# Kernel tuning notes

Hardware: AMD Instinct MI355X
Metric: run time of the kernel (lower is better)

Reference implementation:

```python
import jax, jax.numpy as jnp
import numpy as np

B, S, C = 4, 8192, 256        # batch, seq len, channels
NW, WS, PSZ, D = 2048, 256, 256, 32  # words, word_size, p_size, window radius


def setup_inputs() -> dict:
    key = jax.random.key(0)
    k0, k1, k2, k3, k4 = jax.random.split(key, 5)
    q = jax.random.normal(k0, (B, S, C), jnp.float32)
    c_t = jax.random.normal(k1, (B, NW, WS), jnp.float32)
    # scale weights ~1/sqrt(fan_in) so sigmoid in predictive alignment is not saturated
    W_a = jax.random.normal(k2, (WS, C), jnp.float32) / np.sqrt(C).astype(np.float32)
    W_p = jax.random.normal(k3, (PSZ, WS), jnp.float32) / np.sqrt(WS).astype(np.float32)
    V_p = jax.random.normal(k4, (1, PSZ), jnp.float32) / np.sqrt(PSZ).astype(np.float32)
    return {"q": q, "c_t": c_t, "W_a": W_a, "W_p": W_p, "V_p": V_p}


def reference(q, c_t, W_a, W_p, V_p):
    Bq, Sq, Cq = q.shape
    # predictive alignment: p_t = S * sigmoid(V_p(tanh(W_p(c_t))))  -> [B, NW, 1]
    p_t = Sq * jax.nn.sigmoid(jnp.tanh(c_t @ W_p.T) @ V_p.T)
    # window positions s in [p-D, p+D]; torch .long() truncates (p_t > 0 so == floor)
    offs = jnp.arange(-D, D + 1)                       # [K]
    s = p_t[..., 0].astype(jnp.int32)[:, :, None] + offs  # [B, NW, K]
    # pad a leading NaN row; out-of-range indices map to it (clamp then mod)
    q_pad = jnp.concatenate([jnp.full((Bq, 1, Cq), jnp.nan, q.dtype), q], axis=1)  # [B, S+1, C]
    idx = jnp.clip(s + 1, 0, Sq + 1) % (Sq + 1)        # S+1 wraps to the NaN row (0)
    qw = jax.vmap(lambda qb, ib: qb[ib])(q_pad, idx)   # [B, NW, K, C] gathered windows
    nan_mask = jnp.isnan(qw[..., 0])                   # [B, NW, K]
    qw = jnp.where(nan_mask[..., None], 0.0, qw)       # zero invalid keys (used for output too)
    Wq = qw @ W_a.T                                    # [B, NW, K, WS]
    a_t = jnp.einsum('bwkd,bwd->bwk', Wq, c_t)         # per-window scores
    a_t = jnp.where(nan_mask, -jnp.inf, a_t)           # NaN keys -> -inf before softmax
    prob = jax.nn.softmax(a_t, axis=2)
    # Gaussian truncation around predicted position p_t
    prob = prob * jnp.exp(-2.0 * jnp.square((s.astype(q.dtype) - p_t) / D))
    out = jnp.einsum('bwk,bwkc->bwc', prob, qw)        # [B, NW, C]
    return out
```

## Files before the change

kernel.cpp:

```cpp
#include <hip/hip_runtime.h>
#include <math.h>

#define BB 4
#define S 8192
#define C 256
#define NW 2048
#define WS 256
#define PSZ 256
#define DD 32
#define KK 65
#define TOTW (BB * NW)

#define KC 64
#define LDA 68
#define NBKT 64
#define TBKT (BB * NBKT)

__global__ __launch_bounds__(256) void prep_B(const float* __restrict__ Wp,
                                              const float* __restrict__ Wa,
                                              float* __restrict__ Bp,
                                              int* __restrict__ cnt) {
    const int k = blockIdx.x;
    const int t = threadIdx.x;
    Bp[k * 512 + t] = Wp[t * WS + k];
    Bp[k * 512 + 256 + t] = Wa[k * C + t];
    if (k == 0) cnt[t] = 0;
}

__global__ __launch_bounds__(256, 4) void precomp_gemm(const float* __restrict__ ct,
                                                       const float* __restrict__ Bp,
                                                       const float* __restrict__ Vp,
                                                       float* __restrict__ ptpart,
                                                       float* __restrict__ g) {
    __shared__ __align__(16) float Al[KC][LDA];
    __shared__ __align__(16) float Bl[KC][LDA];

    const int t = threadIdx.x;
    const int bm = blockIdx.x >> 3;
    const int bn = blockIdx.x & 7;
    const int tm = t >> 4;
    const int tn = t & 15;
    const int sm = t >> 2;
    const int sf = t & 3;

    const float4* ct4 = (const float4*)ct;
    const float4* B4  = (const float4*)Bp;

    float acc[4][4] = {{0.f}};

    for (int kc = 0; kc < 256; kc += KC) {
        __syncthreads();
#pragma unroll
        for (int i = 0; i < 4; i++) {
            const float4 a = ct4[(size_t)(bm * 64 + sm) * 64 + (kc >> 2) + sf + i * 4];
            const int kl = (sf + i * 4) * 4;
            Al[kl + 0][sm] = a.x;
            Al[kl + 1][sm] = a.y;
            Al[kl + 2][sm] = a.z;
            Al[kl + 3][sm] = a.w;
        }
#pragma unroll
        for (int i = 0; i < 4; i++) {
            const float4 b = B4[(size_t)(kc + sm) * 128 + bn * 16 + sf + i * 4];
            *(float4*)&Bl[sm][(sf + i * 4) * 4] = b;
        }
        __syncthreads();

#pragma unroll 8
        for (int kk = 0; kk < KC; kk++) {
            const float4 a = *(const float4*)&Al[kk][tm * 4];
            const float4 b = *(const float4*)&Bl[kk][tn * 4];
            acc[0][0] = fmaf(a.x, b.x, acc[0][0]);
            acc[0][1] = fmaf(a.x, b.y, acc[0][1]);
            acc[0][2] = fmaf(a.x, b.z, acc[0][2]);
            acc[0][3] = fmaf(a.x, b.w, acc[0][3]);
            acc[1][0] = fmaf(a.y, b.x, acc[1][0]);
            acc[1][1] = fmaf(a.y, b.y, acc[1][1]);
            acc[1][2] = fmaf(a.y, b.z, acc[1][2]);
            acc[1][3] = fmaf(a.y, b.w, acc[1][3]);
            acc[2][0] = fmaf(a.z, b.x, acc[2][0]);
            acc[2][1] = fmaf(a.z, b.y, acc[2][1]);
            acc[2][2] = fmaf(a.z, b.z, acc[2][2]);
            acc[2][3] = fmaf(a.z, b.w, acc[2][3]);
            acc[3][0] = fmaf(a.w, b.x, acc[3][0]);
            acc[3][1] = fmaf(a.w, b.y, acc[3][1]);
            acc[3][2] = fmaf(a.w, b.z, acc[3][2]);
            acc[3][3] = fmaf(a.w, b.w, acc[3][3]);
        }
    }

    if (bn >= 4) {
        const int col = bn * 64 + tn * 4 - 256;
#pragma unroll
        for (int i = 0; i < 4; i++) {
            const int row = bm * 64 + tm * 4 + i;
            *(float4*)&g[(size_t)row * 256 + col] =
                make_float4(acc[i][0], acc[i][1], acc[i][2], acc[i][3]);
        }
    } else {
        const float4 vp4 = ((const float4*)Vp)[bn * 16 + tn];
#pragma unroll
        for (int i = 0; i < 4; i++) {
            float v = tanhf(acc[i][0]) * vp4.x;
            v = fmaf(tanhf(acc[i][1]), vp4.y, v);
            v = fmaf(tanhf(acc[i][2]), vp4.z, v);
            v = fmaf(tanhf(acc[i][3]), vp4.w, v);
#pragma unroll
            for (int off = 8; off >= 1; off >>= 1) v += __shfl_xor(v, off);
            if (tn == 0) {
                const int row = bm * 64 + tm * 4 + i;
                ptpart[row * 4 + bn] = v;
            }
        }
    }
}

__global__ __launch_bounds__(256) void pt_hist(const float* __restrict__ ptpart,
                                               float* __restrict__ pt,
                                               int* __restrict__ cnt) {
    const int wg = blockIdx.x * 256 + threadIdx.x;
    const float4 pp = ((const float4*)ptpart)[wg];
    const float x = (pp.x + pp.y) + (pp.z + pp.w);
    const float p = (float)S / (1.f + expf(-x));
    pt[wg] = p;
    const int s0 = (int)p;
    const int bkt = (wg >> 11) * NBKT + min(NBKT - 1, max(0, s0 >> 7));
    atomicAdd(&cnt[bkt], 1);
}

__global__ __launch_bounds__(256) void scan_kernel(const int* __restrict__ cnt,
                                                   int* __restrict__ offs) {
    __shared__ int sh[TBKT];
    const int t = threadIdx.x;
    const int v = cnt[t];
    sh[t] = v;
    __syncthreads();
    for (int d = 1; d < TBKT; d <<= 1) {
        const int x = (t >= d) ? sh[t - d] : 0;
        __syncthreads();
        sh[t] += x;
        __syncthreads();
    }
    offs[t] = sh[t] - v;
}

__global__ __launch_bounds__(256) void scatter_kernel(const float* __restrict__ pt,
                                                      int* __restrict__ offs,
                                                      int* __restrict__ perm) {
    const int wg = blockIdx.x * 256 + threadIdx.x;
    const int s0 = (int)pt[wg];
    const int bkt = (wg >> 11) * NBKT + min(NBKT - 1, max(0, s0 >> 7));
    const int pos = atomicAdd(&offs[bkt], 1);
    perm[pos] = wg;
}

__global__ __launch_bounds__(256, 3) void attn(const float* __restrict__ q,
                                               const float* __restrict__ g,
                                               const float* __restrict__ pt,
                                               const int* __restrict__ perm,
                                               float* __restrict__ out) {
    __shared__ __align__(16) float4 accbuf[4][64];
    __shared__ float mbuf[4], dbuf[4];

    const int tid = threadIdx.x;
    const int l = tid & 63;
    const int wv = tid >> 6;
    const int gw = l >> 4;
    const int sub = l & 15;
    const int kslot = tid >> 4;

    const int bid = blockIdx.x;
    const int sb = (bid & 7) * 1024 + (bid >> 3);
    const int wg = perm[sb];
    const int b = wg >> 11;

    const float p = pt[wg];
    const int s0 = (int)p;

    const float* grow = g + (size_t)wg * C + sub * 4;
    const float4 g0 = *(const float4*)(grow);
    const float4 g1 = *(const float4*)(grow + 64);
    const float4 g2 = *(const float4*)(grow + 128);
    const float4 g3 = *(const float4*)(grow + 192);

    const float* qb = q + (size_t)b * S * C + sub * 4;

    float4 qh[5][4];
#pragma unroll
    for (int it = 0; it < 5; it++) {
        const int s = s0 + it * 16 + kslot - DD;
        const float* qr = qb + (size_t)min(max(s, 0), S - 1) * C;
        qh[it][0] = *(const float4*)(qr);
        qh[it][1] = *(const float4*)(qr + 64);
        qh[it][2] = *(const float4*)(qr + 128);
        qh[it][3] = *(const float4*)(qr + 192);
    }

    float e[5];
#pragma unroll
    for (int it = 0; it < 5; it++) {
        const int k = it * 16 + kslot;
        const int s = s0 + k - DD;
        const bool valid = (k <= 64) && ((unsigned)s < (unsigned)S);
        float d0 = qh[it][0].x * g0.x, d1 = qh[it][1].x * g1.x;
        float d2 = qh[it][2].x * g2.x, d3 = qh[it][3].x * g3.x;
        d0 = fmaf(qh[it][0].y, g0.y, d0); d1 = fmaf(qh[it][1].y, g1.y, d1);
        d2 = fmaf(qh[it][2].y, g2.y, d2); d3 = fmaf(qh[it][3].y, g3.y, d3);
        d0 = fmaf(qh[it][0].z, g0.z, d0); d1 = fmaf(qh[it][1].z, g1.z, d1);
        d2 = fmaf(qh[it][2].z, g2.z, d2); d3 = fmaf(qh[it][3].z, g3.z, d3);
        d0 = fmaf(qh[it][0].w, g0.w, d0); d1 = fmaf(qh[it][1].w, g1.w, d1);
        d2 = fmaf(qh[it][2].w, g2.w, d2); d3 = fmaf(qh[it][3].w, g3.w, d3);
        float d = (d0 + d1) + (d2 + d3);
#pragma unroll
        for (int off = 8; off >= 1; off >>= 1) d += __shfl_xor(d, off);
        e[it] = valid ? d : -3e38f;
    }

    float m = e[0];
#pragma unroll
    for (int it = 1; it < 5; it++) m = fmaxf(m, e[it]);
    m = fmaxf(m, __shfl_xor(m, 16));
    m = fmaxf(m, __shfl_xor(m, 32));

    float den = 0.f;
#pragma unroll
    for (int it = 0; it < 5; it++) {
        e[it] = __expf(e[it] - m);
        den += e[it];
    }
    den += __shfl_xor(den, 16);
    den += __shfl_xor(den, 32);

#pragma unroll
    for (int it = 0; it < 5; it++) {
        const float fs = (float)(s0 + it * 16 + kslot - DD) - p;
        const float tt = fs * (1.f / (float)DD);
        e[it] *= __expf(-2.f * tt * tt);
    }

    float4 a0 = {0,0,0,0}, a1 = {0,0,0,0}, a2 = {0,0,0,0}, a3 = {0,0,0,0};
#pragma unroll
    for (int it = 0; it < 5; it++) {
        const float w = e[it];
        a0.x = fmaf(w, qh[it][0].x, a0.x); a0.y = fmaf(w, qh[it][0].y, a0.y);
        a0.z = fmaf(w, qh[it][0].z, a0.z); a0.w = fmaf(w, qh[it][0].w, a0.w);
        a1.x = fmaf(w, qh[it][1].x, a1.x); a1.y = fmaf(w, qh[it][1].y, a1.y);
        a1.z = fmaf(w, qh[it][1].z, a1.z); a1.w = fmaf(w, qh[it][1].w, a1.w);
        a2.x = fmaf(w, qh[it][2].x, a2.x); a2.y = fmaf(w, qh[it][2].y, a2.y);
        a2.z = fmaf(w, qh[it][2].z, a2.z); a2.w = fmaf(w, qh[it][2].w, a2.w);
        a3.x = fmaf(w, qh[it][3].x, a3.x); a3.y = fmaf(w, qh[it][3].y, a3.y);
        a3.z = fmaf(w, qh[it][3].z, a3.z); a3.w = fmaf(w, qh[it][3].w, a3.w);
    }

#define MERGE(v) { v += __shfl_xor(v, 16); v += __shfl_xor(v, 32); }
    MERGE(a0.x) MERGE(a0.y) MERGE(a0.z) MERGE(a0.w)
    MERGE(a1.x) MERGE(a1.y) MERGE(a1.z) MERGE(a1.w)
    MERGE(a2.x) MERGE(a2.y) MERGE(a2.z) MERGE(a2.w)
    MERGE(a3.x) MERGE(a3.y) MERGE(a3.z) MERGE(a3.w)
#undef MERGE

    float4 o = a0;
    if (gw == 1) o = a1;
    else if (gw == 2) o = a2;
    else if (gw == 3) o = a3;
    accbuf[wv][l] = o;
    if (l == 0) { mbuf[wv] = m; dbuf[wv] = den; }
    __syncthreads();

    if (tid < 64) {
        const float M = fmaxf(fmaxf(mbuf[0], mbuf[1]), fmaxf(mbuf[2], mbuf[3]));
        const float sc0 = __expf(mbuf[0] - M);
        const float sc1 = __expf(mbuf[1] - M);
        const float sc2 = __expf(mbuf[2] - M);
        const float sc3 = __expf(mbuf[3] - M);
        const float dtot = dbuf[0]*sc0 + dbuf[1]*sc1 + dbuf[2]*sc2 + dbuf[3]*sc3;
        const float4 v0 = accbuf[0][tid];
        const float4 v1 = accbuf[1][tid];
        const float4 v2 = accbuf[2][tid];
        const float4 v3 = accbuf[3][tid];
        const float r = 1.f / dtot;
        float4 oo;
        oo.x = (v0.x*sc0 + v1.x*sc1 + v2.x*sc2 + v3.x*sc3) * r;
        oo.y = (v0.y*sc0 + v1.y*sc1 + v2.y*sc2 + v3.y*sc3) * r;
        oo.z = (v0.z*sc0 + v1.z*sc1 + v2.z*sc2 + v3.z*sc3) * r;
        oo.w = (v0.w*sc0 + v1.w*sc1 + v2.w*sc2 + v3.w*sc3) * r;
        *(float4*)(out + (size_t)wg * C + tid * 4) = oo;
    }
}

extern "C" void kernel_launch(void* const* d_in, const int* in_sizes, int n_in,
                              void* d_out, int out_size, void* d_ws, size_t ws_size,
                              hipStream_t stream) {
    const float* q  = (const float*)d_in[0];
    const float* ct = (const float*)d_in[1];
    const float* Wa = (const float*)d_in[2];
    const float* Wp = (const float*)d_in[3];
    const float* Vp = (const float*)d_in[4];
    float* out = (float*)d_out;

    char* ws = (char*)d_ws;
    float* Bp     = (float*)ws;
    float* ptpart = (float*)(ws + 524288);
    float* pt     = (float*)(ws + 655360);
    int*   cnt    = (int*)  (ws + 688128);
    int*   offs   = (int*)  (ws + 689152);
    int*   perm   = (int*)  (ws + 690176);
    float* g      = (float*)(ws + 722944);

    prep_B<<<256, 256, 0, stream>>>(Wp, Wa, Bp, cnt);
    precomp_gemm<<<1024, 256, 0, stream>>>(ct, Bp, Vp, ptpart, g);
    pt_hist<<<TOTW / 256, 256, 0, stream>>>(ptpart, pt, cnt);
    scan_kernel<<<1, TBKT, 0, stream>>>(cnt, offs);
    scatter_kernel<<<TOTW / 256, 256, 0, stream>>>(pt, offs, perm);
    attn<<<TOTW, 256, 0, stream>>>(q, g, pt, perm, out);
}
```

Baseline: 88.65 us.

## Fuse histogram, scan and scatter into one single-block sort kernel

Replaces the three bucket-sort kernels (global-atomic histogram, scan, scatter) with one single-workgroup kernel that builds the histogram in LDS, scans it, and scatters the permutation. Global counters and their zeroing in prep_B go away, which removes two kernel launches and the global-atomic traffic. The cost is that 8192 items are now processed by a single block serially. The attention kernel's occupancy hint is also lowered from 3 to 2 blocks per CU, and row pointers are kept in an array, presumably for reuse later in the kernel.

```diff
diff --git a/kernel.cpp b/kernel.cpp
--- a/kernel.cpp
+++ b/kernel.cpp
@@ -18,13 +18,11 @@
 
 __global__ __launch_bounds__(256) void prep_B(const float* __restrict__ Wp,
                                               const float* __restrict__ Wa,
-                                              float* __restrict__ Bp,
-                                              int* __restrict__ cnt) {
+                                              float* __restrict__ Bp) {
     const int k = blockIdx.x;
     const int t = threadIdx.x;
     Bp[k * 512 + t] = Wp[t * WS + k];
     Bp[k * 512 + 256 + t] = Wa[k * C + t];
-    if (k == 0) cnt[t] = 0;
 }
 
 __global__ __launch_bounds__(256, 4) void precomp_gemm(const float* __restrict__ ct,
@@ -115,46 +113,51 @@
     }
 }
 
-__global__ __launch_bounds__(256) void pt_hist(const float* __restrict__ ptpart,
-                                               float* __restrict__ pt,
-                                               int* __restrict__ cnt) {
-    const int wg = blockIdx.x * 256 + threadIdx.x;
-    const float4 pp = ((const float4*)ptpart)[wg];
-    const float x = (pp.x + pp.y) + (pp.z + pp.w);
-    const float p = (float)S / (1.f + expf(-x));
-    pt[wg] = p;
-    const int s0 = (int)p;
-    const int bkt = (wg >> 11) * NBKT + min(NBKT - 1, max(0, s0 >> 7));
-    atomicAdd(&cnt[bkt], 1);
-}
-
-__global__ __launch_bounds__(256) void scan_kernel(const int* __restrict__ cnt,
-                                                   int* __restrict__ offs) {
-    __shared__ int sh[TBKT];
+__global__ __launch_bounds__(256) void sort_all(const float* __restrict__ ptpart,
+                                                float* __restrict__ pt,
+                                                int* __restrict__ perm) {
+    __shared__ int hist[TBKT];
+    __shared__ int scan[TBKT];
+
     const int t = threadIdx.x;
-    const int v = cnt[t];
-    sh[t] = v;
+    hist[t] = 0;
+    __syncthreads();
+
+    int bkt[32];
+#pragma unroll
+    for (int it = 0; it < 32; it++) {
+        const int wg = it * 256 + t;
+        const float4 pp = ((const float4*)ptpart)[wg];
+        const float x = (pp.x + pp.y) + (pp.z + pp.w);
+        const float p = (float)S / (1.f + expf(-x));
+        pt[wg] = p;
+        const int s0 = (int)p;
+        bkt[it] = (wg >> 11) * NBKT + min(NBKT - 1, max(0, s0 >> 7));
+        atomicAdd(&hist[bkt[it]], 1);
+    }
+    __syncthreads();
+
+    int v = hist[t];
+    scan[t] = v;
     __syncthreads();
     for (int d = 1; d < TBKT; d <<= 1) {
-        const int x = (t >= d) ? sh[t - d] : 0;
+        const int x = (t >= d) ? scan[t - d] : 0;
         __syncthreads();
-        sh[t] += x;
+        scan[t] += x;
         __syncthreads();
     }
-    offs[t] = sh[t] - v;
-}
-
-__global__ __launch_bounds__(256) void scatter_kernel(const float* __restrict__ pt,
-                                                      int* __restrict__ offs,
-                                                      int* __restrict__ perm) {
-    const int wg = blockIdx.x * 256 + threadIdx.x;
-    const int s0 = (int)pt[wg];
-    const int bkt = (wg >> 11) * NBKT + min(NBKT - 1, max(0, s0 >> 7));
-    const int pos = atomicAdd(&offs[bkt], 1);
-    perm[pos] = wg;
-}
-
-__global__ __launch_bounds__(256, 3) void attn(const float* __restrict__ q,
+    hist[t] = scan[t] - v;
+    __syncthreads();
+
+#pragma unroll
+    for (int it = 0; it < 32; it++) {
+        const int wg = it * 256 + t;
+        const int pos = atomicAdd(&hist[bkt[it]], 1);
+        perm[pos] = wg;
+    }
+}
+
+__global__ __launch_bounds__(256, 2) void attn(const float* __restrict__ q,
                                                const float* __restrict__ g,
                                                const float* __restrict__ pt,
                                                const int* __restrict__ perm,
@@ -185,15 +188,16 @@
 
     const float* qb = q + (size_t)b * S * C + sub * 4;
 
+    const float* qr[5];
     float4 qh[5][4];
 #pragma unroll
     for (int it = 0; it < 5; it++) {
         const int s = s0 + it * 16 + kslot - DD;
-        const float* qr = qb + (size_t)min(max(s, 0), S - 1) * C;
-        qh[it][0] = *(const float4*)(qr);
-        qh[it][1] = *(const float4*)(qr + 64);
-        qh[it][2] = *(const float4*)(qr + 128);
-        qh[it][3] = *(const float4*)(qr + 192);
+        qr[it] = qb + (size_t)min(max(s, 0), S - 1) * C;
+        qh[it][0] = *(const float4*)(qr[it]);
+        qh[it][1] = *(const float4*)(qr[it] + 64);
+        qh[it][2] = *(const float4*)(qr[it] + 128);
+        qh[it][3] = *(const float4*)(qr[it] + 192);
     }
 
     float e[5];
@@ -302,15 +306,11 @@
     float* Bp     = (float*)ws;
     float* ptpart = (float*)(ws + 524288);
     float* pt     = (float*)(ws + 655360);
-    int*   cnt    = (int*)  (ws + 688128);
-    int*   offs   = (int*)  (ws + 689152);
-    int*   perm   = (int*)  (ws + 690176);
-    float* g      = (float*)(ws + 722944);
-
-    prep_B<<<256, 256, 0, stream>>>(Wp, Wa, Bp, cnt);
+    int*   perm   = (int*)  (ws + 688128);
+    float* g      = (float*)(ws + 720896);
+
+    prep_B<<<256, 256, 0, stream>>>(Wp, Wa, Bp);
     precomp_gemm<<<1024, 256, 0, stream>>>(ct, Bp, Vp, ptpart, g);
-    pt_hist<<<TOTW / 256, 256, 0, stream>>>(ptpart, pt, cnt);
-    scan_kernel<<<1, TBKT, 0, stream>>>(cnt, offs);
-    scatter_kernel<<<TOTW / 256, 256, 0, stream>>>(pt, offs, perm);
+    sort_all<<<1, 256, 0, stream>>>(ptpart, pt, perm);
     attn<<<TOTW, 256, 0, stream>>>(q, g, pt, perm, out);
 }
```

New measurement: 91.87 us. 3.6% more time.

## Stage shared q window span in LDS for chunks of sorted words

Applied to the files above, without the earlier changes.

Makes the position buckets finer (16-row buckets) so sorted words in a chunk lie close together. Each 1024-thread block now handles 16 words: it loads a 128-row span of q into LDS once and serves window rows from LDS, falling back to global memory for rows outside the span or from another batch. The goal is to stop re-reading overlapping q windows from global/L2 for every word. In exchange each block uses a large LDS buffer (about 133 KB), only a few blocks fit per CU, and the four rounds per block are serialised by barriers.

```diff
diff --git a/kernel.cpp b/kernel.cpp
--- a/kernel.cpp
+++ b/kernel.cpp
@@ -1,5 +1,6 @@
 #include <hip/hip_runtime.h>
 #include <math.h>
+#include <limits.h>
 
 #define BB 4
 #define S 8192
@@ -13,8 +14,12 @@
 
 #define KC 64
 #define LDA 68
-#define NBKT 64
+#define NBKT 512
 #define TBKT (BB * NBKT)
+
+#define SPAN 128
+#define RSTR 260
+#define CHUNK 16
 
 __global__ __launch_bounds__(256) void prep_B(const float* __restrict__ Wp,
                                               const float* __restrict__ Wa,
@@ -24,7 +29,7 @@
     const int t = threadIdx.x;
     Bp[k * 512 + t] = Wp[t * WS + k];
     Bp[k * 512 + 256 + t] = Wa[k * C + t];
-    if (k == 0) cnt[t] = 0;
+    if (k < 8) cnt[k * 256 + t] = 0;
 }
 
 __global__ __launch_bounds__(256, 4) void precomp_gemm(const float* __restrict__ ct,
@@ -124,24 +129,29 @@
     const float p = (float)S / (1.f + expf(-x));
     pt[wg] = p;
     const int s0 = (int)p;
-    const int bkt = (wg >> 11) * NBKT + min(NBKT - 1, max(0, s0 >> 7));
+    const int bkt = (wg >> 11) * NBKT + min(NBKT - 1, max(0, s0 >> 4));
     atomicAdd(&cnt[bkt], 1);
 }
 
 __global__ __launch_bounds__(256) void scan_kernel(const int* __restrict__ cnt,
                                                    int* __restrict__ offs) {
-    __shared__ int sh[TBKT];
+    __shared__ int sh[256];
     const int t = threadIdx.x;
-    const int v = cnt[t];
-    sh[t] = v;
+    int v[8];
+    int sum = 0;
+#pragma unroll
+    for (int i = 0; i < 8; i++) { v[i] = cnt[t * 8 + i]; sum += v[i]; }
+    sh[t] = sum;
     __syncthreads();
-    for (int d = 1; d < TBKT; d <<= 1) {
+    for (int d = 1; d < 256; d <<= 1) {
         const int x = (t >= d) ? sh[t - d] : 0;
         __syncthreads();
         sh[t] += x;
         __syncthreads();
     }
-    offs[t] = sh[t] - v;
+    int run = (t > 0) ? sh[t - 1] : 0;
+#pragma unroll
+    for (int i = 0; i < 8; i++) { offs[t * 8 + i] = run; run += v[i]; }
 }
 
 __global__ __launch_bounds__(256) void scatter_kernel(const float* __restrict__ pt,
@@ -149,142 +159,208 @@
                                                       int* __restrict__ perm) {
     const int wg = blockIdx.x * 256 + threadIdx.x;
     const int s0 = (int)pt[wg];
-    const int bkt = (wg >> 11) * NBKT + min(NBKT - 1, max(0, s0 >> 7));
+    const int bkt = (wg >> 11) * NBKT + min(NBKT - 1, max(0, s0 >> 4));
     const int pos = atomicAdd(&offs[bkt], 1);
     perm[pos] = wg;
 }
 
-__global__ __launch_bounds__(256, 3) void attn(const float* __restrict__ q,
-                                               const float* __restrict__ g,
-                                               const float* __restrict__ pt,
-                                               const int* __restrict__ perm,
-                                               float* __restrict__ out) {
-    __shared__ __align__(16) float4 accbuf[4][64];
-    __shared__ float mbuf[4], dbuf[4];
+__global__ __launch_bounds__(1024) void attn(const float* __restrict__ q,
+                                             const float* __restrict__ g,
+                                             const float* __restrict__ pt,
+                                             const int* __restrict__ perm,
+                                             float* __restrict__ out) {
+    __shared__ __align__(16) float qlds[SPAN * RSTR];
+    __shared__ __align__(16) float4 accbuf[4][4][64];
+    __shared__ float mbuf[4][4], dbuf[4][4];
+    __shared__ int wgs[CHUNK];
+    __shared__ float pts[CHUNK];
+    __shared__ int baseSh;
 
     const int tid = threadIdx.x;
+    const int bid = blockIdx.x;
+    const int chunk = (bid & 7) * 64 + (bid >> 3);
+
+    if (tid < CHUNK) {
+        const int w = perm[chunk * CHUNK + tid];
+        wgs[tid] = w;
+        pts[tid] = pt[w];
+    }
+    __syncthreads();
+
+    if (tid == 0) {
+        const int b0 = wgs[0] >> 11;
+        int mn = INT_MAX;
+#pragma unroll
+        for (int i = 0; i < CHUNK; i++)
+            if ((wgs[i] >> 11) == b0) mn = min(mn, (int)pts[i]);
+        int base = mn - DD;
+        baseSh = max(0, min(base, S - SPAN));
+    }
+    __syncthreads();
+
+    const int base = baseSh;
+    const int batch0 = wgs[0] >> 11;
+
+    {
+        const float4* src = (const float4*)(q + ((size_t)batch0 * S + base) * C);
+#pragma unroll
+        for (int i = 0; i < 8; i++) {
+            const int f = tid + i * 1024;
+            const int r = f >> 6, c = f & 63;
+            *(float4*)&qlds[r * RSTR + c * 4] = src[(size_t)r * 64 + c];
+        }
+    }
+    __syncthreads();
+
+    const int grp = tid >> 8;
+    const int t256 = tid & 255;
     const int l = tid & 63;
-    const int wv = tid >> 6;
-    const int gw = l >> 4;
-    const int sub = l & 15;
-    const int kslot = tid >> 4;
-
-    const int bid = blockIdx.x;
-    const int sb = (bid & 7) * 1024 + (bid >> 3);
-    const int wg = perm[sb];
-    const int b = wg >> 11;
-
-    const float p = pt[wg];
-    const int s0 = (int)p;
-
-    const float* grow = g + (size_t)wg * C + sub * 4;
-    const float4 g0 = *(const float4*)(grow);
-    const float4 g1 = *(const float4*)(grow + 64);
-    const float4 g2 = *(const float4*)(grow + 128);
-    const float4 g3 = *(const float4*)(grow + 192);
-
-    const float* qb = q + (size_t)b * S * C + sub * 4;
-
-    float4 qh[5][4];
-#pragma unroll
-    for (int it = 0; it < 5; it++) {
-        const int s = s0 + it * 16 + kslot - DD;
-        const float* qr = qb + (size_t)min(max(s, 0), S - 1) * C;
-        qh[it][0] = *(const float4*)(qr);
-        qh[it][1] = *(const float4*)(qr + 64);
-        qh[it][2] = *(const float4*)(qr + 128);
-        qh[it][3] = *(const float4*)(qr + 192);
-    }
-
-    float e[5];
-#pragma unroll
-    for (int it = 0; it < 5; it++) {
-        const int k = it * 16 + kslot;
-        const int s = s0 + k - DD;
-        const bool valid = (k <= 64) && ((unsigned)s < (unsigned)S);
-        float d0 = qh[it][0].x * g0.x, d1 = qh[it][1].x * g1.x;
-        float d2 = qh[it][2].x * g2.x, d3 = qh[it][3].x * g3.x;
-        d0 = fmaf(qh[it][0].y, g0.y, d0); d1 = fmaf(qh[it][1].y, g1.y, d1);
-        d2 = fmaf(qh[it][2].y, g2.y, d2); d3 = fmaf(qh[it][3].y, g3.y, d3);
-        d0 = fmaf(qh[it][0].z, g0.z, d0); d1 = fmaf(qh[it][1].z, g1.z, d1);
-        d2 = fmaf(qh[it][2].z, g2.z, d2); d3 = fmaf(qh[it][3].z, g3.z, d3);
-        d0 = fmaf(qh[it][0].w, g0.w, d0); d1 = fmaf(qh[it][1].w, g1.w, d1);
-        d2 = fmaf(qh[it][2].w, g2.w, d2); d3 = fmaf(qh[it][3].w, g3.w, d3);
-        float d = (d0 + d1) + (d2 + d3);
-#pragma unroll
-        for (int off = 8; off >= 1; off >>= 1) d += __shfl_xor(d, off);
-        e[it] = valid ? d : -3e38f;
-    }
-
-    float m = e[0];
-#pragma unroll
-    for (int it = 1; it < 5; it++) m = fmaxf(m, e[it]);
-    m = fmaxf(m, __shfl_xor(m, 16));
-    m = fmaxf(m, __shfl_xor(m, 32));
-
-    float den = 0.f;
-#pragma unroll
-    for (int it = 0; it < 5; it++) {
-        e[it] = __expf(e[it] - m);
-        den += e[it];
-    }
-    den += __shfl_xor(den, 16);
-    den += __shfl_xor(den, 32);
-
-#pragma unroll
-    for (int it = 0; it < 5; it++) {
-        const float fs = (float)(s0 + it * 16 + kslot - DD) - p;
-        const float tt = fs * (1.f / (float)DD);
-        e[it] *= __expf(-2.f * tt * tt);
-    }
-
-    float4 a0 = {0,0,0,0}, a1 = {0,0,0,0}, a2 = {0,0,0,0}, a3 = {0,0,0,0};
-#pragma unroll
-    for (int it = 0; it < 5; it++) {
-        const float w = e[it];
-        a0.x = fmaf(w, qh[it][0].x, a0.x); a0.y = fmaf(w, qh[it][0].y, a0.y);
-        a0.z = fmaf(w, qh[it][0].z, a0.z); a0.w = fmaf(w, qh[it][0].w, a0.w);
-        a1.x = fmaf(w, qh[it][1].x, a1.x); a1.y = fmaf(w, qh[it][1].y, a1.y);
-        a1.z = fmaf(w, qh[it][1].z, a1.z); a1.w = fmaf(w, qh[it][1].w, a1.w);
-        a2.x = fmaf(w, qh[it][2].x, a2.x); a2.y = fmaf(w, qh[it][2].y, a2.y);
-        a2.z = fmaf(w, qh[it][2].z, a2.z); a2.w = fmaf(w, qh[it][2].w, a2.w);
-        a3.x = fmaf(w, qh[it][3].x, a3.x); a3.y = fmaf(w, qh[it][3].y, a3.y);
-        a3.z = fmaf(w, qh[it][3].z, a3.z); a3.w = fmaf(w, qh[it][3].w, a3.w);
-    }
+    const int wv = (tid >> 6) & 3;
+    const int gw = (t256 >> 4) & 3;
+    const int sub = t256 & 15;
+    const int kslot = t256 >> 4;
+
+    for (int rnd = 0; rnd < 4; rnd++) {
+        const int widx = rnd * 4 + grp;
+        const int wg = wgs[widx];
+        const float p = pts[widx];
+        const int s0 = (int)p;
+        const int wb = wg >> 11;
+        const bool sameb = (wb == batch0);
+        const float* qg = q + (size_t)wb * S * C + sub * 4;
+
+        const float* grow = g + (size_t)wg * C + sub * 4;
+        const float4 g0 = *(const float4*)(grow);
+        const float4 g1 = *(const float4*)(grow + 64);
+        const float4 g2 = *(const float4*)(grow + 128);
+        const float4 g3 = *(const float4*)(grow + 192);
+
+        float e[5];
+#pragma unroll
+        for (int it = 0; it < 5; it++) {
+            const int k = it * 16 + kslot;
+            const int s = s0 + k - DD;
+            const bool valid = (k <= 64) && ((unsigned)s < (unsigned)S);
+            const int rr = min(max(s, 0), S - 1);
+            const int idx = rr - base;
+            float4 q0, q1, q2, q3;
+            if (sameb && (unsigned)idx < (unsigned)SPAN) {
+                const float* lp = &qlds[idx * RSTR + sub * 4];
+                q0 = *(const float4*)(lp);
+                q1 = *(const float4*)(lp + 64);
+                q2 = *(const float4*)(lp + 128);
+                q3 = *(const float4*)(lp + 192);
+            } else {
+                const float* gp = qg + (size_t)rr * C;
+                q0 = *(const float4*)(gp);
+                q1 = *(const float4*)(gp + 64);
+                q2 = *(const float4*)(gp + 128);
+                q3 = *(const float4*)(gp + 192);
+            }
+            float d0 = q0.x * g0.x, d1 = q1.x * g1.x;
+            float d2 = q2.x * g2.x, d3 = q3.x * g3.x;
+            d0 = fmaf(q0.y, g0.y, d0); d1 = fmaf(q1.y, g1.y, d1);
+            d2 = fmaf(q2.y, g2.y, d2); d3 = fmaf(q3.y, g3.y, d3);
+            d0 = fmaf(q0.z, g0.z, d0); d1 = fmaf(q1.z, g1.z, d1);
+            d2 = fmaf(q2.z, g2.z, d2); d3 = fmaf(q3.z, g3.z, d3);
+            d0 = fmaf(q0.w, g0.w, d0); d1 = fmaf(q1.w, g1.w, d1);
+            d2 = fmaf(q2.w, g2.w, d2); d3 = fmaf(q3.w, g3.w, d3);
+            float d = (d0 + d1) + (d2 + d3);
+#pragma unroll
+            for (int off = 8; off >= 1; off >>= 1) d += __shfl_xor(d, off);
+            e[it] = valid ? d : -3e38f;
+        }
+
+        float m = e[0];
+#pragma unroll
+        for (int it = 1; it < 5; it++) m = fmaxf(m, e[it]);
+        m = fmaxf(m, __shfl_xor(m, 16));
+        m = fmaxf(m, __shfl_xor(m, 32));
+
+        float den = 0.f;
+#pragma unroll
+        for (int it = 0; it < 5; it++) {
+            e[it] = __expf(e[it] - m);
+            den += e[it];
+        }
+        den += __shfl_xor(den, 16);
+        den += __shfl_xor(den, 32);
+
+#pragma unroll
+        for (int it = 0; it < 5; it++) {
+            const float fs = (float)(s0 + it * 16 + kslot - DD) - p;
+            const float tt = fs * (1.f / (float)DD);
+            e[it] *= __expf(-2.f * tt * tt);
+        }
+
+        float4 a0 = {0,0,0,0}, a1 = {0,0,0,0}, a2 = {0,0,0,0}, a3 = {0,0,0,0};
+#pragma unroll
+        for (int it = 0; it < 5; it++) {
+            const int s = s0 + it * 16 + kslot - DD;
+            const int rr = min(max(s, 0), S - 1);
+            const int idx = rr - base;
+            float4 q0, q1, q2, q3;
+            if (sameb && (unsigned)idx < (unsigned)SPAN) {
+                const float* lp = &qlds[idx * RSTR + sub * 4];
+                q0 = *(const float4*)(lp);
+                q1 = *(const float4*)(lp + 64);
+                q2 = *(const float4*)(lp + 128);
+                q3 = *(const float4*)(lp + 192);
+            } else {
+                const float* gp = qg + (size_t)rr * C;
+                q0 = *(const float4*)(gp);
+                q1 = *(const float4*)(gp + 64);
+                q2 = *(const float4*)(gp + 128);
+                q3 = *(const float4*)(gp + 192);
+            }
+            const float w = e[it];
+            a0.x = fmaf(w, q0.x, a0.x); a0.y = fmaf(w, q0.y, a0.y);
+            a0.z = fmaf(w, q0.z, a0.z); a0.w = fmaf(w, q0.w, a0.w);
+            a1.x = fmaf(w, q1.x, a1.x); a1.y = fmaf(w, q1.y, a1.y);
+            a1.z = fmaf(w, q1.z, a1.z); a1.w = fmaf(w, q1.w, a1.w);
+            a2.x = fmaf(w, q2.x, a2.x); a2.y = fmaf(w, q2.y, a2.y);
+            a2.z = fmaf(w, q2.z, a2.z); a2.w = fmaf(w, q2.w, a2.w);
+            a3.x = fmaf(w, q3.x, a3.x); a3.y = fmaf(w, q3.y, a3.y);
+            a3.z = fmaf(w, q3.z, a3.z); a3.w = fmaf(w, q3.w, a3.w);
+        }
 
 #define MERGE(v) { v += __shfl_xor(v, 16); v += __shfl_xor(v, 32); }
-    MERGE(a0.x) MERGE(a0.y) MERGE(a0.z) MERGE(a0.w)
-    MERGE(a1.x) MERGE(a1.y) MERGE(a1.z) MERGE(a1.w)
-    MERGE(a2.x) MERGE(a2.y) MERGE(a2.z) MERGE(a2.w)
-    MERGE(a3.x) MERGE(a3.y) MERGE(a3.z) MERGE(a3.w)
+        MERGE(a0.x) MERGE(a0.y) MERGE(a0.z) MERGE(a0.w)
+        MERGE(a1.x) MERGE(a1.y) MERGE(a1.z) MERGE(a1.w)
+        MERGE(a2.x) MERGE(a2.y) MERGE(a2.z) MERGE(a2.w)
+        MERGE(a3.x) MERGE(a3.y) MERGE(a3.z) MERGE(a3.w)
 #undef MERGE
 
-    float4 o = a0;
-    if (gw == 1) o = a1;
-    else if (gw == 2) o = a2;
-    else if (gw == 3) o = a3;
-    accbuf[wv][l] = o;
-    if (l == 0) { mbuf[wv] = m; dbuf[wv] = den; }
-    __syncthreads();
-
-    if (tid < 64) {
-        const float M = fmaxf(fmaxf(mbuf[0], mbuf[1]), fmaxf(mbuf[2], mbuf[3]));
-        const float sc0 = __expf(mbuf[0] - M);
-        const float sc1 = __expf(mbuf[1] - M);
-        const float sc2 = __expf(mbuf[2] - M);
-        const float sc3 = __expf(mbuf[3] - M);
-        const float dtot = dbuf[0]*sc0 + dbuf[1]*sc1 + dbuf[2]*sc2 + dbuf[3]*sc3;
-        const float4 v0 = accbuf[0][tid];
-        const float4 v1 = accbuf[1][tid];
-        const float4 v2 = accbuf[2][tid];
-        const float4 v3 = accbuf[3][tid];
-        const float r = 1.f / dtot;
-        float4 oo;
-        oo.x = (v0.x*sc0 + v1.x*sc1 + v2.x*sc2 + v3.x*sc3) * r;
-        oo.y = (v0.y*sc0 + v1.y*sc1 + v2.y*sc2 + v3.y*sc3) * r;
-        oo.z = (v0.z*sc0 + v1.z*sc1 + v2.z*sc2 + v3.z*sc3) * r;
-        oo.w = (v0.w*sc0 + v1.w*sc1 + v2.w*sc2 + v3.w*sc3) * r;
-        *(float4*)(out + (size_t)wg * C + tid * 4) = oo;
+        float4 o = a0;
+        if (gw == 1) o = a1;
+        else if (gw == 2) o = a2;
+        else if (gw == 3) o = a3;
+        accbuf[grp][wv][l] = o;
+        if (l == 0) { mbuf[grp][wv] = m; dbuf[grp][wv] = den; }
+        __syncthreads();
+
+        if (t256 < 64) {
+            const float M = fmaxf(fmaxf(mbuf[grp][0], mbuf[grp][1]),
+                                  fmaxf(mbuf[grp][2], mbuf[grp][3]));
+            const float sc0 = __expf(mbuf[grp][0] - M);
+            const float sc1 = __expf(mbuf[grp][1] - M);
+            const float sc2 = __expf(mbuf[grp][2] - M);
+            const float sc3 = __expf(mbuf[grp][3] - M);
+            const float dtot = dbuf[grp][0]*sc0 + dbuf[grp][1]*sc1 +
+                               dbuf[grp][2]*sc2 + dbuf[grp][3]*sc3;
+            const float4 v0 = accbuf[grp][0][t256];
+            const float4 v1 = accbuf[grp][1][t256];
+            const float4 v2 = accbuf[grp][2][t256];
+            const float4 v3 = accbuf[grp][3][t256];
+            const float r = 1.f / dtot;
+            float4 oo;
+            oo.x = (v0.x*sc0 + v1.x*sc1 + v2.x*sc2 + v3.x*sc3) * r;
+            oo.y = (v0.y*sc0 + v1.y*sc1 + v2.y*sc2 + v3.y*sc3) * r;
+            oo.z = (v0.z*sc0 + v1.z*sc1 + v2.z*sc2 + v3.z*sc3) * r;
+            oo.w = (v0.w*sc0 + v1.w*sc1 + v2.w*sc2 + v3.w*sc3) * r;
+            *(float4*)(out + (size_t)wg * C + t256 * 4) = oo;
+        }
+        __syncthreads();
     }
 }
 
@@ -303,14 +379,14 @@
     float* ptpart = (float*)(ws + 524288);
     float* pt     = (float*)(ws + 655360);
     int*   cnt    = (int*)  (ws + 688128);
-    int*   offs   = (int*)  (ws + 689152);
-    int*   perm   = (int*)  (ws + 690176);
-    float* g      = (float*)(ws + 722944);
+    int*   offs   = (int*)  (ws + 696320);
+    int*   perm   = (int*)  (ws + 704512);
+    float* g      = (float*)(ws + 737280);
 
     prep_B<<<256, 256, 0, stream>>>(Wp, Wa, Bp, cnt);
     precomp_gemm<<<1024, 256, 0, stream>>>(ct, Bp, Vp, ptpart, g);
     pt_hist<<<TOTW / 256, 256, 0, stream>>>(ptpart, pt, cnt);
-    scan_kernel<<<1, TBKT, 0, stream>>>(cnt, offs);
+    scan_kernel<<<1, 256, 0, stream>>>(cnt, offs);
     scatter_kernel<<<TOTW / 256, 256, 0, stream>>>(pt, offs, perm);
-    attn<<<TOTW, 256, 0, stream>>>(q, g, pt, perm, out);
-}
+    attn<<<TOTW / CHUNK, 1024, 0, stream>>>(q, g, pt, perm, out);
+}
```

Result: slower. 110.9 us (+25.1%).
